# Optimization experiments

Hardware: AMD Instinct MI355X
Metric: run time of the kernel (lower is better)

Reference implementation:

```python
import jax, jax.numpy as jnp
import numpy as np

N_NODES = 10000
N_EDGES = 160000
MUL = 128          # channel multiplicity
N_SPECIES = 10
SH_OFF = [0, 1, 4, 9, 16]   # spherical-harmonic offsets for l=0..3 (2l+1 each)
RADIAL_IN = 8
SIN_DIM = 32
MAX_DENSITY = 100.0


def setup_inputs() -> dict:
    key = jax.random.key(0)
    ks = jax.random.split(key, 16)
    inp = {
        'node_attrs': jax.random.normal(ks[0], (N_NODES, N_SPECIES), jnp.float32),
        'node_feats': jax.random.normal(ks[1], (N_NODES, MUL), jnp.float32),
        'edge_attrs': jax.random.normal(ks[2], (N_EDGES, 16), jnp.float32),
        'edge_feats': jax.random.normal(ks[3], (N_EDGES, RADIAL_IN), jnp.float32),
        'edge_index': jax.random.randint(ks[4], (2, N_EDGES), 0, N_NODES, jnp.int64),
        'W_up': jax.random.normal(ks[5], (MUL, MUL), jnp.float32),
        'Wr1': jax.random.normal(ks[6], (RADIAL_IN, 64), jnp.float32),
        'Wr2': jax.random.normal(ks[7], (64, 64), jnp.float32),
        'Wr3': jax.random.normal(ks[8], (64, 64), jnp.float32),
        'Wr4': jax.random.normal(ks[9], (64, 4 * MUL), jnp.float32),
        'Wd': jax.random.normal(ks[10], (RADIAL_IN, 1), jnp.float32),
        'Wsin': jax.random.normal(ks[11], (SIN_DIM, MUL), jnp.float32),
        'Wlin': jax.random.normal(ks[12], (4, MUL, MUL), jnp.float32),
        'Wskip': jax.random.normal(ks[13], (4, MUL, N_SPECIES, MUL), jnp.float32),
    }
    return inp


def _sinusoidal_embedding(x):
    # continuous sinusoidal embedding: dim=32, max_density=100
    half = SIN_DIM // 2
    freqs = jnp.exp(-jnp.log(MAX_DENSITY) * jnp.arange(half, dtype=x.dtype) / half)
    ang = x[:, None] * freqs[None, :]          # [N, 16]
    return jnp.concatenate([jnp.sin(ang), jnp.cos(ang)], axis=-1)  # [N, 32]


def reference(node_attrs, node_feats, edge_attrs, edge_feats, edge_index,
              W_up, Wr1, Wr2, Wr3, Wr4, Wd, Wsin, Wlin, Wskip):
    N = node_feats.shape[0]
    sender, receiver = edge_index[0], edge_index[1]

    # linear_up (e3nn o3.Linear on 128x0e, fan-in normalized)
    x = node_feats @ (W_up / np.float32(np.sqrt(MUL)))          # [N, 128]

    # radial MLP: FullyConnectedNet([8,64,64,64,512], silu), fan-in normalized
    h = edge_feats
    for W in (Wr1, Wr2, Wr3):
        h = jax.nn.silu(h @ (W / np.float32(np.sqrt(W.shape[0]))))
    tp_w = (h @ (Wr4 / np.float32(np.sqrt(64)))).reshape(-1, 4, MUL)  # [E, 4, 128]

    # equivariant TP: scalar node feats (x) gathered by sender, uvu path per SH l
    xs = x[sender]                                              # [E, 128]
    weighted = xs[:, None, :] * tp_w                            # [E, 4, 128]
    blocks = []
    for l in range(4):
        sh_l = edge_attrs[:, SH_OFF[l]:SH_OFF[l + 1]]           # [E, 2l+1]
        blk = weighted[:, l, :, None] * sh_l[:, None, :]        # [E, 128, 2l+1]
        blocks.append(blk.reshape(blk.shape[0], -1))
    mji = jnp.concatenate(blocks, axis=-1)                      # [E, 2048]

    # per-edge density gate
    density = jnp.tanh((edge_feats @ Wd) ** 2)                  # [E, 1]

    # scatter-sum messages and density to receivers
    message = jax.ops.segment_sum(mji, receiver, num_segments=N)        # [N, 2048]
    rho = jax.ops.segment_sum(density, receiver, num_segments=N)       # [N, 1]
    message = message / (rho + 1.0)

    # density embedding injected into the l=0 block
    demb = _sinusoidal_embedding(rho[:, 0]) @ Wsin              # [N, 128]
    message = message.at[:, :MUL].add(demb)

    # per-l linear (irreps_mid -> irreps_out), skip_tp with node_attrs, reshape
    out_blocks = []
    for l in range(4):
        d = 2 * l + 1
        blk = message[:, MUL * SH_OFF[l]:MUL * SH_OFF[l + 1]].reshape(N, MUL, d)
        blk = jnp.einsum('nuk,uv->nvk', blk, Wlin[l]) / np.float32(np.sqrt(MUL))
        blk = jnp.einsum('nvk,na,vaw->nwk', blk, node_attrs, Wskip[l]) \
              / np.float32(np.sqrt(MUL * N_SPECIES))
        out_blocks.append(blk)
    return jnp.concatenate(out_blocks, axis=-1)                 # [N, 128, 16]
```

## Files before the change

kernel.cpp:

```cpp
#include <hip/hip_runtime.h>
#include <hip/hip_bf16.h>

#define N_NODES 10000
#define N_EDGES 160000

typedef _Float16 h8 __attribute__((ext_vector_type(8)));
typedef _Float16 h4 __attribute__((ext_vector_type(4)));
typedef float f32x4 __attribute__((ext_vector_type(4)));

__device__ __forceinline__ float silu_f(float v){ return v / (1.f + expf(-v)); }

__global__ __launch_bounds__(256) void k_pre(const float* __restrict__ Wr2,
                                             const float* __restrict__ Wr3,
                                             const float* __restrict__ Wr4,
                                             const float* __restrict__ Wup,
                                             const float* __restrict__ Wlin,
                                             const float* __restrict__ Wskip,
                                             const int* __restrict__ eidx,
                                             _Float16* __restrict__ Wr2T,
                                             _Float16* __restrict__ Wr3T,
                                             _Float16* __restrict__ Wr4T,
                                             _Float16* __restrict__ WupT,
                                             _Float16* __restrict__ WC16T,
                                             int* __restrict__ cnt){
  const int b = blockIdx.x;
  __shared__ float wl[128];
  if (b < 224){
    const int idx = b*256 + threadIdx.x;
    if (idx < 4096){
      const int n = idx >> 6, k = idx & 63;
      Wr2T[idx] = (_Float16)(Wr2[k*64 + n] * 0.125f);
    } else if (idx < 8192){
      const int j = idx - 4096;
      const int n = j >> 6, k = j & 63;
      Wr3T[j] = (_Float16)(Wr3[k*64 + n] * 0.125f);
    } else if (idx < 40960){
      const int j = idx - 8192;
      const int n = j >> 6, k = j & 63;
      Wr4T[j] = (_Float16)(Wr4[k*512 + n] * 0.125f);
    } else if (idx < 57344){
      const int j = idx - 40960;
      const int u = j >> 7, k = j & 127;
      WupT[j] = (_Float16)(Wup[k*128 + u] * 0.08838834764831843f);
    }
  } else if (b < 736){
    const int lu = b - 224;
    const int l  = lu >> 7, u = lu & 127;
    if (threadIdx.x < 128) wl[threadIdx.x] = Wlin[lu*128 + threadIdx.x];
    __syncthreads();
    const float* Wsk = Wskip + (size_t)l * 163840;
    for (int i = threadIdx.x; i < 1280; i += 256){
      float acc = 0.f;
      #pragma unroll 16
      for (int v = 0; v < 128; ++v) acc += wl[v] * Wsk[v*1280 + i];
      const int a = i >> 7, w = i & 127;
      WC16T[((size_t)l*128 + w)*1280 + a*128 + u] =
          (_Float16)(acc * 0.0024705294220065465f);
    }
  } else {
    const int e = (b - 736)*256 + threadIdx.x;
    if (e < N_EDGES) atomicAdd(&cnt[eidx[N_EDGES + e]], 1);
  }
}

__global__ __launch_bounds__(256) void k_scan(const int* __restrict__ cnt,
                                              int* __restrict__ off,
                                              int* __restrict__ cur){
  __shared__ int sums[256];
  const int t = threadIdx.x;
  const int base = t * 40;
  int s = 0;
  for (int i = 0; i < 40; ++i){
    const int idx = base + i;
    if (idx < N_NODES) s += cnt[idx];
  }
  sums[t] = s;
  __syncthreads();
  for (int st = 1; st < 256; st <<= 1){
    const int v = (t >= st) ? sums[t - st] : 0;
    __syncthreads();
    sums[t] += v;
    __syncthreads();
  }
  int pre = (t > 0) ? sums[t - 1] : 0;
  for (int i = 0; i < 40; ++i){
    const int idx = base + i;
    if (idx < N_NODES){
      off[idx] = pre; cur[idx] = pre;
      pre += cnt[idx];
    }
  }
  if (t == 255) off[N_NODES] = sums[255];
}

__global__ __launch_bounds__(256) void k_mid(const int* __restrict__ eidx,
                                             const float* __restrict__ ef,
                                             const float* __restrict__ ea,
                                             int* __restrict__ cur,
                                             int* __restrict__ esnd,
                                             float* __restrict__ efp,
                                             float* __restrict__ eap,
                                             const float* __restrict__ nf,
                                             const _Float16* __restrict__ WupT,
                                             float* __restrict__ x){
  const int b = blockIdx.x;
  const int tid = threadIdx.x;
  alignas(16) __shared__ _Float16 s_nf[64*128];
  alignas(16) __shared__ _Float16 s_wt[128*128];

  if (b < 625){
    const int e = b * 256 + tid;
    if (e < N_EDGES){
      const int pos = atomicAdd(&cur[eidx[N_EDGES + e]], 1);
      esnd[pos] = eidx[e];
      const float4* efs = (const float4*)(ef + (size_t)e*8);
      float4* efd = (float4*)(efp + (size_t)pos*8);
      efd[0] = efs[0]; efd[1] = efs[1];
      const float4* eas = (const float4*)(ea + (size_t)e*16);
      float4* ead = (float4*)(eap + (size_t)pos*16);
      ead[0] = eas[0]; ead[1] = eas[1]; ead[2] = eas[2]; ead[3] = eas[3];
    }
    return;
  }

  const int n0 = (b - 625) * 64;
  {
    const int rl = tid >> 2, part = tid & 3;
    const int gr = n0 + rl;
    #pragma unroll
    for (int j = 0; j < 4; ++j){
      const int cu = part*4 + j;
      h8 hv = (h8){};
      if (gr < N_NODES){
        const float4 v0 = *(const float4*)(nf + (size_t)gr*128 + cu*8);
        const float4 v1 = *(const float4*)(nf + (size_t)gr*128 + cu*8 + 4);
        hv[0]=(_Float16)v0.x; hv[1]=(_Float16)v0.y; hv[2]=(_Float16)v0.z; hv[3]=(_Float16)v0.w;
        hv[4]=(_Float16)v1.x; hv[5]=(_Float16)v1.y; hv[6]=(_Float16)v1.z; hv[7]=(_Float16)v1.w;
      }
      const int cs = (cu & 8) | ((cu & 7) ^ (rl & 7));
      *(h8*)&s_nf[rl*128 + cs*8] = hv;
    }
  }
  {
    const int rl = tid >> 1, part = tid & 1;
    #pragma unroll
    for (int j = 0; j < 8; ++j){
      const int cu = part*8 + j;
      const h8 v = *(const h8*)&WupT[(size_t)rl*128 + cu*8];
      const int cs = (cu & 8) | ((cu & 7) ^ (rl & 7));
      *(h8*)&s_wt[rl*128 + cs*8] = v;
    }
  }
  __syncthreads();

  const int wid = tid >> 6, lane = tid & 63;
  const int li = lane & 15, kg = lane >> 4;

  f32x4 acc[8];
  #pragma unroll
  for (int i = 0; i < 8; ++i) acc[i] = (f32x4){0,0,0,0};

  const int row = wid*16 + li;
  #pragma unroll
  for (int s = 0; s < 4; ++s){
    const int ca = s*4 + kg;
    const int csA = (ca & 8) | ((ca & 7) ^ (row & 7));
    const h8 af = *(const h8*)&s_nf[row*128 + csA*8];
    #pragma unroll
    for (int nt = 0; nt < 8; ++nt){
      const int u = nt*16 + li;
      const int csB = (ca & 8) | ((ca & 7) ^ (u & 7));
      const h8 bf = *(const h8*)&s_wt[u*128 + csB*8];
      acc[nt] = __builtin_amdgcn_mfma_f32_16x16x32_f16(af, bf, acc[nt], 0, 0, 0);
    }
  }
  #pragma unroll
  for (int nt = 0; nt < 8; ++nt){
    #pragma unroll
    for (int r = 0; r < 4; ++r){
      const int gr = n0 + wid*16 + kg*4 + r;
      if (gr < N_NODES) x[(size_t)gr*128 + nt*16 + li] = acc[nt][r];
    }
  }
}

__global__ __launch_bounds__(256) void k_fused(const float* __restrict__ efp,
                                               const float* __restrict__ eap,
                                               const float* __restrict__ x,
                                               const float* __restrict__ Wr1,
                                               const float* __restrict__ Wd,
                                               const _Float16* __restrict__ Wr2T,
                                               const _Float16* __restrict__ Wr3T,
                                               const _Float16* __restrict__ Wr4T,
                                               const float* __restrict__ Wsin,
                                               const int* __restrict__ off,
                                               const int* __restrict__ esnd,
                                               _Float16* __restrict__ msg16){
  const int n0 = blockIdx.x * 4;
  const int tid = threadIdx.x;
  const int lane = tid & 63, wid = tid >> 6;
  const int li = lane & 15, kg = lane >> 4;
  const int u = tid & 127, h = tid >> 7;

  __shared__ float s_ef[2][32][8];
  __shared__ float s_w1[8][64];
  alignas(16) __shared__ _Float16 s_xs[2][32][132];
  alignas(16) __shared__ _Float16 s_actA[32][64];
  alignas(16) __shared__ _Float16 s_actB[32][64];
  alignas(16) __shared__ _Float16 s_w2[32][520];
  alignas(16) __shared__ float s_sh[2][32][16];
  __shared__ float s_dd[32];
  __shared__ float s_rho[4];
  __shared__ int   s_offs[5];
  __shared__ float s_emb[4][32];

  if (tid < 5) s_offs[tid] = off[n0 + tid];
  if (tid < 4) s_rho[tid] = 0.f;
  for (int j = tid; j < 512; j += 256) s_w1[j >> 6][j & 63] = Wr1[j];
  __syncthreads();

  const int beg = s_offs[0], end = s_offs[4];
  const int ngrp = (end - beg + 31) >> 5;

  const int e8 = tid >> 3, i8 = tid & 7;
  const int slotB = tid >> 4, jjB = tid & 15;

  float a0[8] = {0,0,0,0,0,0,0,0};
  float a1[8] = {0,0,0,0,0,0,0,0};
  float a2[8] = {0,0,0,0,0,0,0,0};
  float a3[8] = {0,0,0,0,0,0,0,0};

  if (ngrp > 0){
    const int p = beg + e8;
    s_ef[0][e8][i8] = (p < end) ? efp[(size_t)p*8 + i8] : 0.f;
    const int pB0 = beg + slotB, pB1 = beg + slotB + 16;
    s_sh[0][slotB][jjB]      = (pB0 < end) ? eap[(size_t)pB0*16 + jjB] : 0.f;
    s_sh[0][slotB + 16][jjB] = (pB1 < end) ? eap[(size_t)pB1*16 + jjB] : 0.f;
    const int snd = (p < end) ? esnd[p] : 0;
    const float4* xp = (const float4*)(x + (size_t)snd*128 + i8*16);
    #pragma unroll
    for (int j = 0; j < 4; ++j){
      const float4 v = xp[j];
      h4 hv; hv[0]=(_Float16)v.x; hv[1]=(_Float16)v.y; hv[2]=(_Float16)v.z; hv[3]=(_Float16)v.w;
      *(h4*)&s_xs[0][e8][i8*16 + j*4] = hv;
    }
  }
  __syncthreads();

  for (int g = 0; g < ngrp; ++g){
    const int cur = g & 1, nxt = cur ^ 1;
    const int pbase  = beg + g*32;
    const int pbase2 = pbase + 32;
    const bool more = (g + 1 < ngrp);

    float ef_r = 0.f, sh_r0 = 0.f, sh_r1 = 0.f;
    int snd_r = 0;
    const int pA = pbase2 + e8;
    const bool vA = more && (pA < end);
    if (vA){ ef_r = efp[(size_t)pA*8 + i8]; snd_r = esnd[pA]; }
    const int pB0 = pbase2 + slotB, pB1 = pbase2 + slotB + 16;
    if (more && pB0 < end) sh_r0 = eap[(size_t)pB0*16 + jjB];
    if (more && pB1 < end) sh_r1 = eap[(size_t)pB1*16 + jjB];

    if (tid < 32){
      float s = 0.f;
      #pragma unroll
      for (int i = 0; i < 8; ++i) s += s_ef[cur][tid][i] * Wd[i];
      s_dd[tid] = tanhf(s*s);
    }

    {
      const int e = tid >> 3, ng = tid & 7;
      float hv[8] = {0,0,0,0,0,0,0,0};
      #pragma unroll
      for (int k = 0; k < 8; ++k){
        const float ev = s_ef[cur][e][k] * 0.3535533905932738f;
        #pragma unroll
        for (int j = 0; j < 8; ++j) hv[j] += ev * s_w1[k][ng*8 + j];
      }
      h8 o;
      #pragma unroll
      for (int j = 0; j < 8; ++j) o[j] = (_Float16)silu_f(hv[j]);
      *(h8*)&s_actA[e][(ng ^ (e & 7))*8] = o;
    }
    __syncthreads();

    {
      h8 af[2];
      #pragma unroll
      for (int s = 0; s < 2; ++s)
        af[s] = *(const h8*)&Wr2T[(size_t)(wid*16 + li)*64 + s*32 + kg*8];
      #pragma unroll
      for (int nt = 0; nt < 2; ++nt){
        const int e = nt*16 + li;
        f32x4 acc = (f32x4){0,0,0,0};
        #pragma unroll
        for (int s = 0; s < 2; ++s){
          const h8 bf = *(const h8*)&s_actA[e][((s*4 + kg) ^ (e & 7))*8];
          acc = __builtin_amdgcn_mfma_f32_16x16x32_f16(af[s], bf, acc, 0, 0, 0);
        }
        #pragma unroll
        for (int r = 0; r < 4; ++r){
          const int n = wid*16 + kg*4 + r;
          s_actB[e][((n >> 3) ^ (e & 7))*8 + (n & 7)] = (_Float16)silu_f(acc[r]);
        }
      }
    }
    __syncthreads();

    float4 xs_r0 = {0,0,0,0}, xs_r1 = {0,0,0,0}, xs_r2 = {0,0,0,0}, xs_r3 = {0,0,0,0};
    if (vA){
      const float4* xp = (const float4*)(x + (size_t)snd_r*128 + i8*16);
      xs_r0 = xp[0]; xs_r1 = xp[1]; xs_r2 = xp[2]; xs_r3 = xp[3];
    }

    {
      h8 af[2];
      #pragma unroll
      for (int s = 0; s < 2; ++s)
        af[s] = *(const h8*)&Wr3T[(size_t)(wid*16 + li)*64 + s*32 + kg*8];
      #pragma unroll
      for (int nt = 0; nt < 2; ++nt){
        const int e = nt*16 + li;
        f32x4 acc = (f32x4){0,0,0,0};
        #pragma unroll
        for (int s = 0; s < 2; ++s){
          const h8 bf = *(const h8*)&s_actB[e][((s*4 + kg) ^ (e & 7))*8];
          acc = __builtin_amdgcn_mfma_f32_16x16x32_f16(af[s], bf, acc, 0, 0, 0);
        }
        #pragma unroll
        for (int r = 0; r < 4; ++r){
          const int n = wid*16 + kg*4 + r;
          s_actA[e][((n >> 3) ^ (e & 7))*8 + (n & 7)] = (_Float16)silu_f(acc[r]);
        }
      }
    }
    __syncthreads();

    {
      h8 bf[2][2];
      #pragma unroll
      for (int nt = 0; nt < 2; ++nt){
        const int e = nt*16 + li;
        #pragma unroll
        for (int s = 0; s < 2; ++s)
          bf[nt][s] = *(const h8*)&s_actA[e][((s*4 + kg) ^ (e & 7))*8];
      }
      #pragma unroll
      for (int p = 0; p < 2; ++p){
        #pragma unroll
        for (int mt = 0; mt < 4; ++mt){
          const int nbase = wid*128 + p*64 + mt*16;
          h8 af[2];
          #pragma unroll
          for (int s = 0; s < 2; ++s)
            af[s] = *(const h8*)&Wr4T[(size_t)(nbase + li)*64 + s*32 + kg*8];
          f32x4 acc[2];
          #pragma unroll
          for (int nt = 0; nt < 2; ++nt){
            acc[nt] = (f32x4){0,0,0,0};
            #pragma unroll
            for (int s = 0; s < 2; ++s)
              acc[nt] = __builtin_amdgcn_mfma_f32_16x16x32_f16(af[s], bf[nt][s], acc[nt], 0, 0, 0);
          }
          const int c0 = nbase + kg*4;
          const int u0 = c0 & 127;
          #pragma unroll
          for (int nt = 0; nt < 2; ++nt){
            const int e = nt*16 + li;
            const h4 xv = *(const h4*)&s_xs[cur][e][u0];
            h4 ov;
            #pragma unroll
            for (int r = 0; r < 4; ++r) ov[r] = (_Float16)acc[nt][r] * xv[r];
            *(h4*)&s_w2[e][c0] = ov;
          }
        }
      }
    }
    __syncthreads();

    int lo0 = s_offs[0] - pbase; lo0 = lo0 < 0 ? 0 : lo0;
    int hi0 = s_offs[1] - pbase; hi0 = hi0 > 32 ? 32 : (hi0 < 0 ? 0 : hi0);
    int lo1 = s_offs[1] - pbase; lo1 = lo1 < 0 ? 0 : lo1;
    int hi1 = s_offs[2] - pbase; hi1 = hi1 > 32 ? 32 : (hi1 < 0 ? 0 : hi1);
    int lo2 = s_offs[2] - pbase; lo2 = lo2 < 0 ? 0 : lo2;
    int hi2 = s_offs[3] - pbase; hi2 = hi2 > 32 ? 32 : (hi2 < 0 ? 0 : hi2);
    int lo3 = s_offs[3] - pbase; lo3 = lo3 < 0 ? 0 : lo3;
    int hi3 = s_offs[4] - pbase; hi3 = hi3 > 32 ? 32 : (hi3 < 0 ? 0 : hi3);

#define ACC_H0(A, LO, HI)                                            \
    for (int s = (LO); s < (HI); ++s){                               \
      const float wa  = (float)s_w2[s][u];                           \
      const float wb  = (float)s_w2[s][128 + u];                     \
      const float wcv = (float)s_w2[s][256 + u];                     \
      const float4 sa = *(const float4*)&s_sh[cur][s][0];            \
      const float4 sb = *(const float4*)&s_sh[cur][s][4];            \
      A[0] += wa*sa.x;                                               \
      A[1] += wb*sa.y;  A[2] += wb*sa.z;  A[3] += wb*sa.w;           \
      A[4] += wcv*sb.x; A[5] += wcv*sb.y;                            \
      A[6] += wcv*sb.z; A[7] += wcv*sb.w;                            \
    }
#define ACC_H1(A, LO, HI)                                            \
    for (int s = (LO); s < (HI); ++s){                               \
      const float wcv = (float)s_w2[s][256 + u];                     \
      const float wd  = (float)s_w2[s][384 + u];                     \
      const float4 sa = *(const float4*)&s_sh[cur][s][8];            \
      const float4 sb = *(const float4*)&s_sh[cur][s][12];           \
      A[0] += wcv*sa.x;                                              \
      A[1] += wd*sa.y;  A[2] += wd*sa.z;  A[3] += wd*sa.w;           \
      A[4] += wd*sb.x;  A[5] += wd*sb.y;                             \
      A[6] += wd*sb.z;  A[7] += wd*sb.w;                             \
    }

    if (h == 0){
      ACC_H0(a0, lo0, hi0) ACC_H0(a1, lo1, hi1)
      ACC_H0(a2, lo2, hi2) ACC_H0(a3, lo3, hi3)
    } else {
      ACC_H1(a0, lo0, hi0) ACC_H1(a1, lo1, hi1)
      ACC_H1(a2, lo2, hi2) ACC_H1(a3, lo3, hi3)
    }

    if (tid < 4){
      int lo = s_offs[tid]     - pbase; lo = lo < 0 ? 0 : lo;
      int hi = s_offs[tid + 1] - pbase; hi = hi > 32 ? 32 : (hi < 0 ? 0 : hi);
      float r = 0.f;
      for (int s = lo; s < hi; ++s) r += s_dd[s];
      s_rho[tid] += r;
    }

    if (more){
      s_ef[nxt][e8][i8] = ef_r;
      s_sh[nxt][slotB][jjB]      = sh_r0;
      s_sh[nxt][slotB + 16][jjB] = sh_r1;
      const float4 xr[4] = {xs_r0, xs_r1, xs_r2, xs_r3};
      #pragma unroll
      for (int j = 0; j < 4; ++j){
        h4 hv; hv[0]=(_Float16)xr[j].x; hv[1]=(_Float16)xr[j].y;
        hv[2]=(_Float16)xr[j].z; hv[3]=(_Float16)xr[j].w;
        *(h4*)&s_xs[nxt][e8][i8*16 + j*4] = hv;
      }
    }
    __syncthreads();
  }

  if (tid < 64){
    const int ni = tid >> 4, f = tid & 15;
    const float fr  = expf(-0.28782313662425572f * (float)f);
    const float ang = s_rho[ni] * fr;
    s_emb[ni][f]      = sinf(ang);
    s_emb[ni][f + 16] = cosf(ang);
  }
  __syncthreads();

  float db0 = 0.f, db1 = 0.f, db2 = 0.f, db3 = 0.f;
  if (h == 0){
    #pragma unroll 8
    for (int j = 0; j < 32; ++j){
      const float wsv = Wsin[j*128 + u];
      db0 += s_emb[0][j]*wsv; db1 += s_emb[1][j]*wsv;
      db2 += s_emb[2][j]*wsv; db3 += s_emb[3][j]*wsv;
    }
  }
  const float t0 = 1.f/(s_rho[0]+1.f), t1 = 1.f/(s_rho[1]+1.f);
  const float t2 = 1.f/(s_rho[2]+1.f), t3 = 1.f/(s_rho[3]+1.f);
  #pragma unroll
  for (int j = 0; j < 8; ++j){
    float v0 = a0[j]*t0, v1 = a1[j]*t1, v2 = a2[j]*t2, v3 = a3[j]*t3;
    if (h == 0 && j == 0){ v0 += db0; v1 += db1; v2 += db2; v3 += db3; }
    const size_t base = (size_t)(h*8 + j)*128 + u;
    msg16[(size_t)(n0+0)*2048 + base] = (_Float16)v0;
    msg16[(size_t)(n0+1)*2048 + base] = (_Float16)v1;
    msg16[(size_t)(n0+2)*2048 + base] = (_Float16)v2;
    msg16[(size_t)(n0+3)*2048 + base] = (_Float16)v3;
  }
}

template<int L, int D>
__device__ __forceinline__ void final_body(const int bb,
                                           const _Float16* __restrict__ msg16,
                                           const float* __restrict__ attrs,
                                           const _Float16* __restrict__ WC16T,
                                           float* __restrict__ outD,
                                           _Float16* __restrict__ sA,
                                           _Float16* __restrict__ sB,
                                           _Float16* __restrict__ sAttr){
  constexpr int OFF  = (L==0 ? 0 : L==1 ? 1 : L==2 ? 4 : 9);
  constexpr int ROWS = N_NODES * D;
  const int r0  = bb * 128;
  const int tid = threadIdx.x;

  {
    const int rl = tid >> 2, quarter = tid & 3;
    const int gr = r0 + rl;
    h8 vals[4];
    if (gr < ROWS){
      const int n = gr / D, k = gr - n*D;
      const _Float16* src = msg16 + (size_t)n*2048 + (size_t)(OFF+k)*128 + quarter*32;
      #pragma unroll
      for (int j = 0; j < 4; ++j) vals[j] = *(const h8*)(src + j*8);
    } else {
      #pragma unroll
      for (int j = 0; j < 4; ++j) vals[j] = (h8){};
    }
    #pragma unroll
    for (int j = 0; j < 4; ++j){
      const int cu = quarter*4 + j;
      const int cs = (cu & 8) | ((cu & 7) ^ (rl & 7));
      *(h8*)&sA[rl*128 + cs*8] = vals[j];
    }
  }
  for (int i = tid; i < 1280; i += 512){
    const int rl = i / 10, aa = i - rl*10;
    const int gr = r0 + rl;
    sAttr[i] = (gr < ROWS) ? (_Float16)attrs[(gr / D)*10 + aa] : (_Float16)0.f;
  }
  {
    const int w = tid >> 2, part = tid & 3;
    const _Float16* src = WC16T + ((size_t)L*128 + w)*1280 + part*16;
    #pragma unroll
    for (int j = 0; j < 2; ++j){
      const h8 v = *(const h8*)(src + j*8);
      const int cc = part*2 + j;
      *(h8*)&sB[w*64 + (cc ^ (w & 7))*8] = v;
    }
  }
  __syncthreads();

  const int wid = tid >> 6, lane = tid & 63;
  const int wm = wid >> 2, wn = wid & 3;
  const int li = lane & 15, kg = lane >> 4;

  f32x4 acc[4][2];
  #pragma unroll
  for (int m = 0; m < 4; ++m)
    #pragma unroll
    for (int nn = 0; nn < 2; ++nn) acc[m][nn] = (f32x4){0,0,0,0};

  for (int step = 0; step < 20; ++step){
    _Float16* sbc = (step & 1) ? (sB + 8192) : sB;
    _Float16* sbn = (step & 1) ? sB : (sB + 8192);
    const bool more = (step + 1 < 20);
    h8 pre[2];
    if (more){
      const int a2 = (step+1) >> 1, u02 = ((step+1) & 1) << 6;
      const _Float16* src = WC16T + ((size_t)L*128 + (tid>>2))*1280 + a2*128 + u02 + (tid&3)*16;
      #pragma unroll
      for (int j = 0; j < 2; ++j) pre[j] = *(const h8*)(src + j*8);
    }

    const int a  = step >> 1;
    const int uh = (step & 1) << 3;

    h8 afr[4][2], bfr[2][2];
    #pragma unroll
    for (int m = 0; m < 4; ++m){
      const int row = wm*64 + m*16 + li;
      const _Float16 av = sAttr[row*10 + a];
      h8 avx;
      #pragma unroll
      for (int j = 0; j < 8; ++j) avx[j] = av;
      #pragma unroll
      for (int s = 0; s < 2; ++s){
        const int ca = uh + s*4 + kg;
        const int cs = (ca & 8) | ((ca & 7) ^ (row & 7));
        const h8 mA = *(const h8*)&sA[row*128 + cs*8];
        afr[m][s] = mA * avx;
      }
    }
    #pragma unroll
    for (int nn = 0; nn < 2; ++nn){
      const int w = wn*32 + nn*16 + li;
      #pragma unroll
      for (int s = 0; s < 2; ++s){
        const int cb = s*4 + kg;
        bfr[nn][s] = *(const h8*)&sbc[w*64 + ((cb ^ (w & 7)))*8];
      }
    }
    #pragma unroll
    for (int s = 0; s < 2; ++s)
      #pragma unroll
      for (int m = 0; m < 4; ++m)
        #pragma unroll
        for (int nn = 0; nn < 2; ++nn)
          acc[m][nn] = __builtin_amdgcn_mfma_f32_16x16x32_f16(afr[m][s], bfr[nn][s], acc[m][nn], 0, 0, 0);

    if (more){
      const int w = tid >> 2, part = tid & 3;
      #pragma unroll
      for (int j = 0; j < 2; ++j){
        const int cc = part*2 + j;
        *(h8*)&sbn[w*64 + (cc ^ (w & 7))*8] = pre[j];
      }
    }
    __syncthreads();
  }

  #pragma unroll
  for (int m = 0; m < 4; ++m){
    const int rbase = r0 + wm*64 + m*16 + kg*4;
    #pragma unroll
    for (int rr = 0; rr < 4; ++rr){
      const int gr = rbase + rr;
      if (gr < ROWS){
        float* op = outD + (size_t)gr*128;
        #pragma unroll
        for (int nn = 0; nn < 2; ++nn)
          op[wn*32 + nn*16 + li] = acc[m][nn][rr];
      }
    }
  }
}

__global__ __launch_bounds__(512) void k_final_all(const _Float16* __restrict__ msg16,
                                                   const float* __restrict__ attrs,
                                                   const _Float16* __restrict__ WC16T,
                                                   float* __restrict__ outD){
  alignas(16) __shared__ _Float16 sA[128*128];
  alignas(16) __shared__ _Float16 sB[2*64*128];
  __shared__ _Float16 sAttr[128*10];
  const int b = blockIdx.x;
  if (b < 79)       final_body<0,1>(b,       msg16, attrs, WC16T, outD,            sA, sB, sAttr);
  else if (b < 314) final_body<1,3>(b - 79,  msg16, attrs, WC16T, outD + 1280000,  sA, sB, sAttr);
  else if (b < 705) final_body<2,5>(b - 314, msg16, attrs, WC16T, outD + 5120000,  sA, sB, sAttr);
  else              final_body<3,7>(b - 705, msg16, attrs, WC16T, outD + 11520000, sA, sB, sAttr);
}

__global__ __launch_bounds__(256) void k_merge(const float* __restrict__ outD,
                                               float* __restrict__ out){
  const int n0 = blockIdx.x * 4;
  const int tid = threadIdx.x;
  __shared__ float lds[4*16*132];

  {
    const float4* src = (const float4*)(outD + (size_t)n0*128);
    for (int j = tid; j < 128; j += 256){
      const int row = j >> 5, c4 = j & 31;
      *(float4*)&lds[(row*16 + 0)*132 + c4*4] = src[j];
    }
  }
  {
    const float4* src = (const float4*)(outD + 1280000 + (size_t)n0*3*128);
    for (int j = tid; j < 384; j += 256){
      const int row = j >> 5, c4 = j & 31;
      const int nloc = row/3, k = row - nloc*3;
      *(float4*)&lds[(nloc*16 + 1 + k)*132 + c4*4] = src[j];
    }
  }
  {
    const float4* src = (const float4*)(outD + 5120000 + (size_t)n0*5*128);
    for (int j = tid; j < 640; j += 256){
      const int row = j >> 5, c4 = j & 31;
      const int nloc = row/5, k = row - nloc*5;
      *(float4*)&lds[(nloc*16 + 4 + k)*132 + c4*4] = src[j];
    }
  }
  {
    const float4* src = (const float4*)(outD + 11520000 + (size_t)n0*7*128);
    for (int j = tid; j < 896; j += 256){
      const int row = j >> 5, c4 = j & 31;
      const int nloc = row/7, k = row - nloc*7;
      *(float4*)&lds[(nloc*16 + 9 + k)*132 + c4*4] = src[j];
    }
  }
  __syncthreads();

  for (int j = tid; j < 2048; j += 256){
    const int nloc = j >> 9, qv = j & 511;
    const int w = qv >> 2, s0 = (qv & 3) << 2;
    float4 v;
    v.x = lds[(nloc*16 + s0 + 0)*132 + w];
    v.y = lds[(nloc*16 + s0 + 1)*132 + w];
    v.z = lds[(nloc*16 + s0 + 2)*132 + w];
    v.w = lds[(nloc*16 + s0 + 3)*132 + w];
    *(float4*)&out[(size_t)(n0 + nloc)*2048 + qv*4] = v;
  }
}

extern "C" void kernel_launch(void* const* d_in, const int* in_sizes, int n_in,
                              void* d_out, int out_size, void* d_ws, size_t ws_size,
                              hipStream_t stream){
  const float* node_attrs = (const float*)d_in[0];
  const float* node_feats = (const float*)d_in[1];
  const float* edge_attrs = (const float*)d_in[2];
  const float* edge_feats = (const float*)d_in[3];
  const int*   edge_index = (const int*)d_in[4];
  const float* W_up  = (const float*)d_in[5];
  const float* Wr1   = (const float*)d_in[6];
  const float* Wr2   = (const float*)d_in[7];
  const float* Wr3   = (const float*)d_in[8];
  const float* Wr4   = (const float*)d_in[9];
  const float* Wd    = (const float*)d_in[10];
  const float* Wsin  = (const float*)d_in[11];
  const float* Wlin  = (const float*)d_in[12];
  const float* Wskip = (const float*)d_in[13];
  float* out = (float*)d_out;

  float* outD     = (float*)d_ws;
  _Float16* msg16 = (_Float16*)(outD + 20480000);
  float* x        = (float*)(msg16 + 20480000);
  _Float16* WC16T = (_Float16*)(x + 1280000);
  int* cnt   = (int*)(WC16T + 655360);
  int* off   = cnt + 10000;
  int* cur   = off + 10016;
  int* esnd  = cur + 10000;
  float* efp = (float*)(esnd + 160000);
  float* eap = efp + 1280000;
  _Float16* Wr2T = (_Float16*)(eap + 2560000);
  _Float16* Wr3T = Wr2T + 4096;
  _Float16* Wr4T = Wr3T + 4096;
  _Float16* WupT = Wr4T + 32768;

  hipMemsetAsync(cnt, 0, (size_t)10000 * sizeof(int), stream);

  k_pre<<<1361, 256, 0, stream>>>(Wr2, Wr3, Wr4, W_up, Wlin, Wskip, edge_index,
                                  Wr2T, Wr3T, Wr4T, WupT, WC16T, cnt);
  k_scan<<<1, 256, 0, stream>>>(cnt, off, cur);
  k_mid<<<782, 256, 0, stream>>>(edge_index, edge_feats, edge_attrs,
                                 cur, esnd, efp, eap,
                                 node_feats, WupT, x);

  k_fused<<<N_NODES/4, 256, 0, stream>>>(efp, eap, x,
                                         Wr1, Wd, Wr2T, Wr3T, Wr4T, Wsin,
                                         off, esnd, msg16);

  k_final_all<<<1252, 512, 0, stream>>>(msg16, node_attrs, WC16T, outD);

  k_merge<<<2500, 256, 0, stream>>>(outD, out);
}
```

Baseline: 310.6 us.

## Split Wr4 weight stage into two passes and store intermediate output in fp16

The fused edge kernel now computes the 512-wide per-edge tensor-product weights in two 256-wide passes, halving the s_w2 shared buffer and single-buffering s_ef/s_xs. This lowers LDS use per block, which could raise occupancy, at the cost of an extra barrier per group. Separately, the per-l final GEMM output staged in workspace is stored as fp16 instead of fp32 and converted back in the merge kernel, halving that intermediate traffic but adding rounding error.

```diff
diff --git a/kernel.cpp b/kernel.cpp
--- a/kernel.cpp
+++ b/kernel.cpp
@@ -202,12 +202,12 @@
   const int li = lane & 15, kg = lane >> 4;
   const int u = tid & 127, h = tid >> 7;
 
-  __shared__ float s_ef[2][32][8];
+  __shared__ float s_ef[32][8];
   __shared__ float s_w1[8][64];
-  alignas(16) __shared__ _Float16 s_xs[2][32][132];
+  alignas(16) __shared__ _Float16 s_xs[32][132];
   alignas(16) __shared__ _Float16 s_actA[32][64];
   alignas(16) __shared__ _Float16 s_actB[32][64];
-  alignas(16) __shared__ _Float16 s_w2[32][520];
+  alignas(16) __shared__ _Float16 s_w2[32][264];
   alignas(16) __shared__ float s_sh[2][32][16];
   __shared__ float s_dd[32];
   __shared__ float s_rho[4];
@@ -232,7 +232,7 @@
 
   if (ngrp > 0){
     const int p = beg + e8;
-    s_ef[0][e8][i8] = (p < end) ? efp[(size_t)p*8 + i8] : 0.f;
+    s_ef[e8][i8] = (p < end) ? efp[(size_t)p*8 + i8] : 0.f;
     const int pB0 = beg + slotB, pB1 = beg + slotB + 16;
     s_sh[0][slotB][jjB]      = (pB0 < end) ? eap[(size_t)pB0*16 + jjB] : 0.f;
     s_sh[0][slotB + 16][jjB] = (pB1 < end) ? eap[(size_t)pB1*16 + jjB] : 0.f;
@@ -242,7 +242,7 @@
     for (int j = 0; j < 4; ++j){
       const float4 v = xp[j];
       h4 hv; hv[0]=(_Float16)v.x; hv[1]=(_Float16)v.y; hv[2]=(_Float16)v.z; hv[3]=(_Float16)v.w;
-      *(h4*)&s_xs[0][e8][i8*16 + j*4] = hv;
+      *(h4*)&s_xs[e8][i8*16 + j*4] = hv;
     }
   }
   __syncthreads();
@@ -265,7 +265,7 @@
     if (tid < 32){
       float s = 0.f;
       #pragma unroll
-      for (int i = 0; i < 8; ++i) s += s_ef[cur][tid][i] * Wd[i];
+      for (int i = 0; i < 8; ++i) s += s_ef[tid][i] * Wd[i];
       s_dd[tid] = tanhf(s*s);
     }
 
@@ -274,7 +274,7 @@
       float hv[8] = {0,0,0,0,0,0,0,0};
       #pragma unroll
       for (int k = 0; k < 8; ++k){
-        const float ev = s_ef[cur][e][k] * 0.3535533905932738f;
+        const float ev = s_ef[e][k] * 0.3535533905932738f;
         #pragma unroll
         for (int j = 0; j < 8; ++j) hv[j] += ev * s_w1[k][ng*8 + j];
       }
@@ -284,6 +284,8 @@
       *(h8*)&s_actA[e][(ng ^ (e & 7))*8] = o;
     }
     __syncthreads();
+
+    if (more) s_ef[e8][i8] = ef_r;
 
     {
       h8 af[2];
@@ -332,48 +334,6 @@
         for (int r = 0; r < 4; ++r){
           const int n = wid*16 + kg*4 + r;
           s_actA[e][((n >> 3) ^ (e & 7))*8 + (n & 7)] = (_Float16)silu_f(acc[r]);
-        }
-      }
-    }
-    __syncthreads();
-
-    {
-      h8 bf[2][2];
-      #pragma unroll
-      for (int nt = 0; nt < 2; ++nt){
-        const int e = nt*16 + li;
-        #pragma unroll
-        for (int s = 0; s < 2; ++s)
-          bf[nt][s] = *(const h8*)&s_actA[e][((s*4 + kg) ^ (e & 7))*8];
-      }
-      #pragma unroll
-      for (int p = 0; p < 2; ++p){
-        #pragma unroll
-        for (int mt = 0; mt < 4; ++mt){
-          const int nbase = wid*128 + p*64 + mt*16;
-          h8 af[2];
-          #pragma unroll
-          for (int s = 0; s < 2; ++s)
-            af[s] = *(const h8*)&Wr4T[(size_t)(nbase + li)*64 + s*32 + kg*8];
-          f32x4 acc[2];
-          #pragma unroll
-          for (int nt = 0; nt < 2; ++nt){
-            acc[nt] = (f32x4){0,0,0,0};
-            #pragma unroll
-            for (int s = 0; s < 2; ++s)
-              acc[nt] = __builtin_amdgcn_mfma_f32_16x16x32_f16(af[s], bf[nt][s], acc[nt], 0, 0, 0);
-          }
-          const int c0 = nbase + kg*4;
-          const int u0 = c0 & 127;
-          #pragma unroll
-          for (int nt = 0; nt < 2; ++nt){
-            const int e = nt*16 + li;
-            const h4 xv = *(const h4*)&s_xs[cur][e][u0];
-            h4 ov;
-            #pragma unroll
-            for (int r = 0; r < 4; ++r) ov[r] = (_Float16)acc[nt][r] * xv[r];
-            *(h4*)&s_w2[e][c0] = ov;
-          }
         }
       }
     }
@@ -388,22 +348,34 @@
     int lo3 = s_offs[3] - pbase; lo3 = lo3 < 0 ? 0 : lo3;
     int hi3 = s_offs[4] - pbase; hi3 = hi3 > 32 ? 32 : (hi3 < 0 ? 0 : hi3);
 
-#define ACC_H0(A, LO, HI)                                            \
+    h8 bf[2][2];
+    #pragma unroll
+    for (int nt = 0; nt < 2; ++nt){
+      const int e = nt*16 + li;
+      #pragma unroll
+      for (int s = 0; s < 2; ++s)
+        bf[nt][s] = *(const h8*)&s_actA[e][((s*4 + kg) ^ (e & 7))*8];
+    }
+
+#define ACCA(A, LO, HI)                                              \
     for (int s = (LO); s < (HI); ++s){                               \
       const float wa  = (float)s_w2[s][u];                           \
       const float wb  = (float)s_w2[s][128 + u];                     \
-      const float wcv = (float)s_w2[s][256 + u];                     \
       const float4 sa = *(const float4*)&s_sh[cur][s][0];            \
-      const float4 sb = *(const float4*)&s_sh[cur][s][4];            \
       A[0] += wa*sa.x;                                               \
       A[1] += wb*sa.y;  A[2] += wb*sa.z;  A[3] += wb*sa.w;           \
+    }
+#define ACCB0(A, LO, HI)                                             \
+    for (int s = (LO); s < (HI); ++s){                               \
+      const float wcv = (float)s_w2[s][u];                           \
+      const float4 sb = *(const float4*)&s_sh[cur][s][4];            \
       A[4] += wcv*sb.x; A[5] += wcv*sb.y;                            \
       A[6] += wcv*sb.z; A[7] += wcv*sb.w;                            \
     }
-#define ACC_H1(A, LO, HI)                                            \
+#define ACCB1(A, LO, HI)                                             \
     for (int s = (LO); s < (HI); ++s){                               \
-      const float wcv = (float)s_w2[s][256 + u];                     \
-      const float wd  = (float)s_w2[s][384 + u];                     \
+      const float wcv = (float)s_w2[s][u];                           \
+      const float wd  = (float)s_w2[s][128 + u];                     \
       const float4 sa = *(const float4*)&s_sh[cur][s][8];            \
       const float4 sb = *(const float4*)&s_sh[cur][s][12];           \
       A[0] += wcv*sa.x;                                              \
@@ -412,35 +384,72 @@
       A[6] += wd*sb.z;  A[7] += wd*sb.w;                             \
     }
 
-    if (h == 0){
-      ACC_H0(a0, lo0, hi0) ACC_H0(a1, lo1, hi1)
-      ACC_H0(a2, lo2, hi2) ACC_H0(a3, lo3, hi3)
-    } else {
-      ACC_H1(a0, lo0, hi0) ACC_H1(a1, lo1, hi1)
-      ACC_H1(a2, lo2, hi2) ACC_H1(a3, lo3, hi3)
-    }
-
-    if (tid < 4){
-      int lo = s_offs[tid]     - pbase; lo = lo < 0 ? 0 : lo;
-      int hi = s_offs[tid + 1] - pbase; hi = hi > 32 ? 32 : (hi < 0 ? 0 : hi);
-      float r = 0.f;
-      for (int s = lo; s < hi; ++s) r += s_dd[s];
-      s_rho[tid] += r;
-    }
-
-    if (more){
-      s_ef[nxt][e8][i8] = ef_r;
-      s_sh[nxt][slotB][jjB]      = sh_r0;
-      s_sh[nxt][slotB + 16][jjB] = sh_r1;
-      const float4 xr[4] = {xs_r0, xs_r1, xs_r2, xs_r3};
-      #pragma unroll
-      for (int j = 0; j < 4; ++j){
-        h4 hv; hv[0]=(_Float16)xr[j].x; hv[1]=(_Float16)xr[j].y;
-        hv[2]=(_Float16)xr[j].z; hv[3]=(_Float16)xr[j].w;
-        *(h4*)&s_xs[nxt][e8][i8*16 + j*4] = hv;
-      }
-    }
-    __syncthreads();
+    #pragma unroll
+    for (int pass = 0; pass < 2; ++pass){
+      #pragma unroll
+      for (int mt = 0; mt < 4; ++mt){
+        const int cc0 = wid*64 + mt*16;
+        const int nb  = pass*256 + cc0;
+        h8 af[2];
+        #pragma unroll
+        for (int s = 0; s < 2; ++s)
+          af[s] = *(const h8*)&Wr4T[(size_t)(nb + li)*64 + s*32 + kg*8];
+        f32x4 acc[2];
+        #pragma unroll
+        for (int nt = 0; nt < 2; ++nt){
+          acc[nt] = (f32x4){0,0,0,0};
+          #pragma unroll
+          for (int s = 0; s < 2; ++s)
+            acc[nt] = __builtin_amdgcn_mfma_f32_16x16x32_f16(af[s], bf[nt][s], acc[nt], 0, 0, 0);
+        }
+        const int cc = cc0 + kg*4;
+        const int u0 = cc & 127;
+        #pragma unroll
+        for (int nt = 0; nt < 2; ++nt){
+          const int e = nt*16 + li;
+          const h4 xv = *(const h4*)&s_xs[e][u0];
+          h4 ov;
+          #pragma unroll
+          for (int r = 0; r < 4; ++r) ov[r] = (_Float16)acc[nt][r] * xv[r];
+          *(h4*)&s_w2[e][cc] = ov;
+        }
+      }
+      __syncthreads();
+
+      if (pass == 0){
+        if (h == 0){
+          ACCA(a0, lo0, hi0) ACCA(a1, lo1, hi1)
+          ACCA(a2, lo2, hi2) ACCA(a3, lo3, hi3)
+        }
+      } else {
+        if (h == 0){
+          ACCB0(a0, lo0, hi0) ACCB0(a1, lo1, hi1)
+          ACCB0(a2, lo2, hi2) ACCB0(a3, lo3, hi3)
+        } else {
+          ACCB1(a0, lo0, hi0) ACCB1(a1, lo1, hi1)
+          ACCB1(a2, lo2, hi2) ACCB1(a3, lo3, hi3)
+        }
+        if (tid < 4){
+          int lo = s_offs[tid]     - pbase; lo = lo < 0 ? 0 : lo;
+          int hi = s_offs[tid + 1] - pbase; hi = hi > 32 ? 32 : (hi < 0 ? 0 : hi);
+          float r = 0.f;
+          for (int s = lo; s < hi; ++s) r += s_dd[s];
+          s_rho[tid] += r;
+        }
+        if (more){
+          s_sh[nxt][slotB][jjB]      = sh_r0;
+          s_sh[nxt][slotB + 16][jjB] = sh_r1;
+          const float4 xr[4] = {xs_r0, xs_r1, xs_r2, xs_r3};
+          #pragma unroll
+          for (int j = 0; j < 4; ++j){
+            h4 hv; hv[0]=(_Float16)xr[j].x; hv[1]=(_Float16)xr[j].y;
+            hv[2]=(_Float16)xr[j].z; hv[3]=(_Float16)xr[j].w;
+            *(h4*)&s_xs[e8][i8*16 + j*4] = hv;
+          }
+        }
+      }
+      __syncthreads();
+    }
   }
 
   if (tid < 64){
@@ -480,7 +489,7 @@
                                            const _Float16* __restrict__ msg16,
                                            const float* __restrict__ attrs,
                                            const _Float16* __restrict__ WC16T,
-                                           float* __restrict__ outD,
+                                           _Float16* __restrict__ outD,
                                            _Float16* __restrict__ sA,
                                            _Float16* __restrict__ sB,
                                            _Float16* __restrict__ sAttr){
@@ -602,10 +611,10 @@
     for (int rr = 0; rr < 4; ++rr){
       const int gr = rbase + rr;
       if (gr < ROWS){
-        float* op = outD + (size_t)gr*128;
+        _Float16* op = outD + (size_t)gr*128;
         #pragma unroll
         for (int nn = 0; nn < 2; ++nn)
-          op[wn*32 + nn*16 + li] = acc[m][nn][rr];
+          op[wn*32 + nn*16 + li] = (_Float16)acc[m][nn][rr];
       }
     }
   }
@@ -614,7 +623,7 @@
 __global__ __launch_bounds__(512) void k_final_all(const _Float16* __restrict__ msg16,
                                                    const float* __restrict__ attrs,
                                                    const _Float16* __restrict__ WC16T,
-                                                   float* __restrict__ outD){
+                                                   _Float16* __restrict__ outD){
   alignas(16) __shared__ _Float16 sA[128*128];
   alignas(16) __shared__ _Float16 sB[2*64*128];
   __shared__ _Float16 sAttr[128*10];
@@ -625,43 +634,28 @@
   else              final_body<3,7>(b - 705, msg16, attrs, WC16T, outD + 11520000, sA, sB, sAttr);
 }
 
-__global__ __launch_bounds__(256) void k_merge(const float* __restrict__ outD,
+__global__ __launch_bounds__(256) void k_merge(const _Float16* __restrict__ outD,
                                                float* __restrict__ out){
   const int n0 = blockIdx.x * 4;
   const int tid = threadIdx.x;
   __shared__ float lds[4*16*132];
 
-  {
-    const float4* src = (const float4*)(outD + (size_t)n0*128);
-    for (int j = tid; j < 128; j += 256){
-      const int row = j >> 5, c4 = j & 31;
-      *(float4*)&lds[(row*16 + 0)*132 + c4*4] = src[j];
-    }
-  }
-  {
-    const float4* src = (const float4*)(outD + 1280000 + (size_t)n0*3*128);
-    for (int j = tid; j < 384; j += 256){
-      const int row = j >> 5, c4 = j & 31;
-      const int nloc = row/3, k = row - nloc*3;
-      *(float4*)&lds[(nloc*16 + 1 + k)*132 + c4*4] = src[j];
-    }
-  }
-  {
-    const float4* src = (const float4*)(outD + 5120000 + (size_t)n0*5*128);
-    for (int j = tid; j < 640; j += 256){
-      const int row = j >> 5, c4 = j & 31;
-      const int nloc = row/5, k = row - nloc*5;
-      *(float4*)&lds[(nloc*16 + 4 + k)*132 + c4*4] = src[j];
-    }
-  }
-  {
-    const float4* src = (const float4*)(outD + 11520000 + (size_t)n0*7*128);
-    for (int j = tid; j < 896; j += 256){
-      const int row = j >> 5, c4 = j & 31;
-      const int nloc = row/7, k = row - nloc*7;
-      *(float4*)&lds[(nloc*16 + 9 + k)*132 + c4*4] = src[j];
-    }
-  }
+#define MERGE_LOAD(SRC, CHUNKS, ROWS_PER_N, SKOFF)                       \
+  { const _Float16* src = (SRC);                                         \
+    for (int j = tid; j < (CHUNKS); j += 256){                           \
+      const int row = j >> 4, c8 = j & 15;                               \
+      const int nloc = row / (ROWS_PER_N), k = row - nloc*(ROWS_PER_N);  \
+      const h8 v = *(const h8*)(src + (size_t)row*128 + c8*8);           \
+      float* dst = &lds[(nloc*16 + (SKOFF) + k)*132 + c8*8];             \
+      dst[0]=(float)v[0]; dst[1]=(float)v[1]; dst[2]=(float)v[2];        \
+      dst[3]=(float)v[3]; dst[4]=(float)v[4]; dst[5]=(float)v[5];        \
+      dst[6]=(float)v[6]; dst[7]=(float)v[7];                            \
+    } }
+
+  MERGE_LOAD(outD + (size_t)n0*128,                 64,  1, 0)
+  MERGE_LOAD(outD + 1280000 + (size_t)n0*3*128,    192,  3, 1)
+  MERGE_LOAD(outD + 5120000 + (size_t)n0*5*128,    320,  5, 4)
+  MERGE_LOAD(outD + 11520000 + (size_t)n0*7*128,   448,  7, 9)
   __syncthreads();
 
   for (int j = tid; j < 2048; j += 256){
@@ -695,8 +689,8 @@
   const float* Wskip = (const float*)d_in[13];
   float* out = (float*)d_out;
 
-  float* outD     = (float*)d_ws;
-  _Float16* msg16 = (_Float16*)(outD + 20480000);
+  _Float16* outD  = (_Float16*)d_ws;
+  _Float16* msg16 = outD + 20480000;
   float* x        = (float*)(msg16 + 20480000);
   _Float16* WC16T = (_Float16*)(x + 1280000);
   int* cnt   = (int*)(WC16T + 655360);
```

Measured after the change: 315.0 us. No clear change (+1.4%).
